# Kernel optimization log

Hardware: AMD Instinct MI355X
Metric: run time of the kernel (lower is better)

Reference implementation:

```python
import jax, jax.numpy as jnp
import numpy as np

B, S, H, D = 2, 2048, 16, 128
HID = H * D
THETA = 10000.0
SCALE = 1.0 / np.sqrt(D)


def setup_inputs() -> dict:
    key = jax.random.key(0)
    k1, k2, k3 = jax.random.split(key, 3)
    x = jax.random.normal(k1, (B, S, HID), dtype=jnp.float32)
    w_qkv = jax.random.normal(k2, (3 * HID, HID), dtype=jnp.float32) * 0.02
    w_o = jax.random.normal(k3, (HID, HID), dtype=jnp.float32) * 0.02
    return {"x": x, "w_qkv": w_qkv, "w_o": w_o}


def _rope_cos_sin(seq_len, dim, dtype):
    inv_freq = 1.0 / (THETA ** (jnp.arange(0, dim, 2, dtype=jnp.float32) / dim))
    pos = jnp.arange(seq_len, dtype=jnp.float32)
    freqs = pos[:, None] * inv_freq[None, :]          # (S, D/2)
    emb = jnp.concatenate([freqs, freqs], axis=-1)    # (S, D)
    return jnp.cos(emb).astype(dtype), jnp.sin(emb).astype(dtype)


def _rotate_half(t):
    t1, t2 = jnp.split(t, 2, axis=-1)
    return jnp.concatenate([-t2, t1], axis=-1)


def reference(x, w_qkv, w_o):
    b, s, _ = x.shape
    qkv = jnp.einsum('bsh,oh->bso', x, w_qkv)                 # (B,S,3*HID)
    qkv = qkv.reshape(b, s, 3, H, D).transpose(2, 0, 3, 1, 4)  # (3,B,H,S,D)
    q, k, v = qkv[0], qkv[1], qkv[2]
    cos, sin = _rope_cos_sin(s, D, x.dtype)                    # (S,D)
    q = q * cos + _rotate_half(q) * sin
    k = k * cos + _rotate_half(k) * sin
    scores = jnp.einsum('bhqd,bhkd->bhqk', q, k) * SCALE       # (B,H,S,S)
    causal = jnp.triu(jnp.ones((s, s), dtype=bool), k=1)
    scores = jnp.where(causal[None, None], -jnp.inf, scores)
    attn = jax.nn.softmax(scores.astype(jnp.float32), axis=-1).astype(q.dtype)
    out = jnp.einsum('bhqk,bhkd->bhqd', attn, v)               # (B,H,S,D)
    out = out.transpose(0, 2, 1, 3).reshape(b, s, HID)
    return jnp.einsum('bsh,oh->bso', out, w_o)
```

## Files before the change

kernel.cpp:

```cpp
#include <hip/hip_runtime.h>
#include <hip/hip_bf16.h>

typedef unsigned short u16;
typedef unsigned long long u64;
typedef u16 us8 __attribute__((ext_vector_type(8)));
typedef __bf16 bf8_t __attribute__((ext_vector_type(8)));
typedef float f32x4 __attribute__((ext_vector_type(4)));

__device__ __forceinline__ float b2f(u16 u) {
    return __uint_as_float(((unsigned int)u) << 16);
}
__device__ __forceinline__ u16 f2b(float f) {
    union { __hip_bfloat16 h; u16 u; } v;
    v.h = __float2bfloat16(f);
    return v.u;
}
__device__ __forceinline__ f32x4 mfma16(bf8_t a, bf8_t b, f32x4 c) {
    return __builtin_amdgcn_mfma_f32_16x16x32_bf16(a, b, c, 0, 0, 0);
}
__device__ __forceinline__ void gload_lds16(const u16* g, u16* lds_base) {
    __builtin_amdgcn_global_load_lds((const __attribute__((address_space(1))) unsigned int*)g,
                                     (__attribute__((address_space(3))) unsigned int*)lds_base,
                                     16, 0, 0);
}

__global__ __launch_bounds__(256) void f32_to_bf16(const float* __restrict__ src,
                                                   u16* __restrict__ dst, int n8) {
    int idx = blockIdx.x * 256 + threadIdx.x;
    if (idx >= n8) return;
    float4 f0 = ((const float4*)src)[idx * 2];
    float4 f1 = ((const float4*)src)[idx * 2 + 1];
    us8 o;
    o[0] = f2b(f0.x); o[1] = f2b(f0.y); o[2] = f2b(f0.z); o[3] = f2b(f0.w);
    o[4] = f2b(f1.x); o[5] = f2b(f1.y); o[6] = f2b(f1.z); o[7] = f2b(f1.w);
    ((us8*)dst)[idx] = o;
}

#define BARX() __builtin_amdgcn_s_barrier()
#define LGKM0() do { asm volatile("s_waitcnt lgkmcnt(0)" ::: "memory"); \
                     __builtin_amdgcn_sched_barrier(0); } while (0)
#define VM4A()  do { asm volatile("s_waitcnt vmcnt(4)" ::: "memory"); \
                     __builtin_amdgcn_sched_barrier(0); } while (0)

__global__ __launch_bounds__(512, 2) void gemm192(const u16* __restrict__ A,
                                                  const u16* __restrict__ B,
                                                  u16* __restrict__ Cout, int ldc) {
    __shared__ u16 LA[2][256 * 64];
    __shared__ u16 LB[2][192 * 64];

    const int tid = threadIdx.x;
    const int w = tid >> 6, lane = tid & 63;
    const int lm = lane & 15, lq = lane >> 4;
    const int wm = w >> 1, wn = w & 1;

    const int bid = blockIdx.x;
    const int nper = gridDim.x >> 3;
    const int wg = (bid & 7) * nper + (bid >> 3);
    const int mt = wg & 15, nt = wg >> 4;
    const int m0 = mt * 256, n0 = nt * 192;

    const int srow = lane >> 3;
    const int scol = ((lane & 7) ^ srow) * 8;

    const u16* Ag = A + (size_t)(m0 + srow) * 2048 + scol;
    const u16* Bg = B + (size_t)(n0 + srow) * 2048 + scol;

#define STAGE_A2(c, kt, jb) do { \
    _Pragma("unroll") \
    for (int j = 0; j < 2; j++) { \
        int R = ((jb) + j) * 64 + w * 8; \
        gload_lds16(Ag + (size_t)R * 2048 + (kt) * 64, &LA[c][R * 64]); \
    } } while (0)

#define STAGE_B3(c, kt) do { \
    _Pragma("unroll") \
    for (int j = 0; j < 3; j++) { \
        int R = j * 64 + w * 8; \
        gload_lds16(Bg + (size_t)R * 2048 + (kt) * 64, &LB[c][R * 64]); \
    } } while (0)

    bf8_t af[4][2], bfr[6][2];
    f32x4 acc[4][6] = {};
    const int cswz = (lm & 7) << 4;

#define RD_A4(c) do { \
    _Pragma("unroll") \
    for (int m = 0; m < 4; m++) \
    _Pragma("unroll") \
    for (int ks = 0; ks < 2; ks++) { \
        int row = wm * 64 + m * 16 + lm; \
        int o = (row * 128 + ks * 64 + lq * 16) ^ cswz; \
        af[m][ks] = *(const bf8_t*)((const char*)&LA[c][0] + o); \
    } } while (0)

#define RD_B2(c, np) do { \
    _Pragma("unroll") \
    for (int n = 0; n < 2; n++) \
    _Pragma("unroll") \
    for (int ks = 0; ks < 2; ks++) { \
        int row = wn * 96 + ((np) * 2 + n) * 16 + lm; \
        int o = (row * 128 + ks * 64 + lq * 16) ^ cswz; \
        bfr[(np) * 2 + n][ks] = *(const bf8_t*)((const char*)&LB[c][0] + o); \
    } } while (0)

#define QUAD6(np) do { \
    __builtin_amdgcn_s_setprio(1); \
    _Pragma("unroll") \
    for (int m = 0; m < 4; m++) \
    _Pragma("unroll") \
    for (int n = 0; n < 2; n++) \
    _Pragma("unroll") \
    for (int ks = 0; ks < 2; ks++) \
        acc[m][(np) * 2 + n] = mfma16(af[m][ks], bfr[(np) * 2 + n][ks], \
                                      acc[m][(np) * 2 + n]); \
    __builtin_amdgcn_s_setprio(0); \
    } while (0)

#define TILE192(c, tB, tA) do { \
    RD_A4(c); RD_B2(c, 0); \
    STAGE_B3((c) ^ 1, tB); \
    BARX(); LGKM0(); \
    QUAD6(0); \
    BARX(); \
    RD_B2(c, 1); \
    STAGE_A2(c, tA, 0); \
    BARX(); LGKM0(); \
    QUAD6(1); \
    BARX(); \
    RD_B2(c, 2); \
    STAGE_A2(c, tA, 2); \
    BARX(); LGKM0(); \
    QUAD6(2); \
    VM4A(); \
    BARX(); \
} while (0)

    STAGE_A2(0, 0, 0); STAGE_A2(0, 0, 2);
    STAGE_B3(0, 0);
    STAGE_A2(1, 1, 0); STAGE_A2(1, 1, 2);
    VM4A();
    BARX();

    for (int it = 0; it < 16; it++) {
        const int t0 = 2 * it, t1 = 2 * it + 1;
        const int tB0 = t1;
        const int tA0 = (t0 + 2 < 32) ? t0 + 2 : 31;
        const int tB1 = (t1 + 1 < 32) ? t1 + 1 : 31;
        const int tA1 = (t1 + 2 < 32) ? t1 + 2 : 31;
        TILE192(0, tB0, tA0);
        TILE192(1, tB1, tA1);
    }

#pragma unroll
    for (int m = 0; m < 4; m++)
#pragma unroll
        for (int n = 0; n < 6; n++)
#pragma unroll
            for (int r = 0; r < 4; r++) {
                int row = m0 + wm * 64 + m * 16 + lq * 4 + r;
                int col = n0 + wn * 96 + n * 16 + lm;
                Cout[(size_t)row * ldc + col] = f2b(acc[m][n][r]);
            }
#undef TILE192
#undef QUAD6
#undef RD_A4
#undef RD_B2
#undef STAGE_A2
#undef STAGE_B3
}

#define VMN() do { \
    asm volatile("s_waitcnt vmcnt(2)" ::: "memory"); \
    __builtin_amdgcn_sched_barrier(0); } while (0)

__global__ __launch_bounds__(512, 2) void gemm_op(const u16* __restrict__ A,
                                                  const u16* __restrict__ B,
                                                  float* __restrict__ Cout, int ldc) {
    __shared__ u16 LA[2][128 * 64];
    __shared__ u16 LB[2][256 * 64];

    const int tid = threadIdx.x;
    const int w = tid >> 6, lane = tid & 63;
    const int lm = lane & 15, lq = lane >> 4;
    const int wm = w >> 2, wn = w & 3;

    const int bid = blockIdx.x;
    const int nper = gridDim.x >> 3;
    const int wg = (bid & 7) * nper + (bid >> 3);
    const int mt = wg & 31, nt = wg >> 5;
    const int m0 = mt * 128, n0 = nt * 256;

    const int srow = lane >> 3;
    const int scol = ((lane & 7) ^ srow) * 8;

    const u16* Ag = A + (size_t)(m0 + srow) * 2048 + scol;
    const u16* Bg = B + (size_t)(n0 + srow) * 2048 + scol;

#define STAGE_A(c, h, kt) do { \
    _Pragma("unroll") \
    for (int i = 0; i < 2; i++) { \
        int R = w * 2 + i; \
        if ((h) == 0) \
            gload_lds16(Ag + (size_t)(R * 8) * 2048 + (kt) * 64, &LA[c][(R * 8) * 64]); \
    } } while (0)

#define STAGE_B(c, h, kt) do { \
    _Pragma("unroll") \
    for (int i = 0; i < 2; i++) { \
        int R = w * 2 + i; \
        gload_lds16(Bg + (size_t)((h) * 128 + R * 8) * 2048 + (kt) * 64, \
                    &LB[c][((h) * 128 + R * 8) * 64]); \
    } } while (0)

    bf8_t af[4][2], bfr[4][2];
    f32x4 acc[4][4] = {};
    const int cswz = (lm & 7) << 4;

#define RD_A(c, mh) do { \
    _Pragma("unroll") \
    for (int m = 0; m < 2; m++) \
    _Pragma("unroll") \
    for (int ks = 0; ks < 2; ks++) { \
        int row = wm * 64 + ((mh) * 2 + m) * 16 + lm; \
        int o = (row * 128 + ks * 64 + lq * 16) ^ cswz; \
        af[(mh) * 2 + m][ks] = *(const bf8_t*)((const char*)&LA[c][0] + o); \
    } } while (0)

#define RD_B(c, nh) do { \
    _Pragma("unroll") \
    for (int n = 0; n < 2; n++) \
    _Pragma("unroll") \
    for (int ks = 0; ks < 2; ks++) { \
        int row = wn * 64 + ((nh) * 2 + n) * 16 + lm; \
        int o = (row * 128 + ks * 64 + lq * 16) ^ cswz; \
        bfr[(nh) * 2 + n][ks] = *(const bf8_t*)((const char*)&LB[c][0] + o); \
    } } while (0)

#define QUAD(mh, nh) do { \
    __builtin_amdgcn_s_setprio(1); \
    _Pragma("unroll") \
    for (int m = 0; m < 2; m++) \
    _Pragma("unroll") \
    for (int n = 0; n < 2; n++) \
    _Pragma("unroll") \
    for (int ks = 0; ks < 2; ks++) \
        acc[(mh) * 2 + m][(nh) * 2 + n] = mfma16(af[(mh) * 2 + m][ks], \
            bfr[(nh) * 2 + n][ks], acc[(mh) * 2 + m][(nh) * 2 + n]); \
    __builtin_amdgcn_s_setprio(0); \
    } while (0)

#define TILEOP(c, tB, tA) do { \
    RD_A(c, 0); RD_B(c, 0); \
    STAGE_B((c) ^ 1, 0, tB); \
    BARX(); LGKM0(); \
    QUAD(0, 0); \
    BARX(); \
    RD_A(c, 1); \
    STAGE_B((c) ^ 1, 1, tB); \
    BARX(); LGKM0(); \
    QUAD(1, 0); \
    BARX(); \
    RD_B(c, 1); \
    STAGE_A(c, 0, tA); \
    BARX(); LGKM0(); \
    QUAD(0, 1); \
    BARX(); \
    QUAD(1, 1); \
    VMN(); \
    BARX(); \
} while (0)

    STAGE_A(0, 0, 0);
    STAGE_B(0, 0, 0); STAGE_B(0, 1, 0);
    STAGE_A(1, 0, 1);
    VMN();
    BARX();

    for (int it = 0; it < 16; it++) {
        const int t0 = 2 * it, t1 = 2 * it + 1;
        const int tB0 = t1;
        const int tA0 = (t0 + 2 < 32) ? t0 + 2 : 31;
        const int tB1 = (t1 + 1 < 32) ? t1 + 1 : 31;
        const int tA1 = (t1 + 2 < 32) ? t1 + 2 : 31;
        TILEOP(0, tB0, tA0);
        TILEOP(1, tB1, tA1);
    }

#pragma unroll
    for (int m = 0; m < 4; m++)
#pragma unroll
        for (int n = 0; n < 4; n++)
#pragma unroll
            for (int r = 0; r < 4; r++) {
                int row = m0 + wm * 64 + m * 16 + lq * 4 + r;
                int col = n0 + wn * 64 + n * 16 + lm;
                Cout[(size_t)row * ldc + col] = acc[m][n][r];
            }
#undef TILEOP
#undef QUAD
#undef RD_A
#undef RD_B
#undef STAGE_A
#undef STAGE_B
}

__global__ __launch_bounds__(256) void rope_vt(u16* __restrict__ qkv, u16* __restrict__ VT) {
    __shared__ u16 T[64 * 136];
    const int tid = threadIdx.x;
    const int s0 = blockIdx.x * 64;
    const int bh = blockIdx.y;
    const int b = bh >> 4, h = bh & 15;
#pragma unroll
    for (int p = 0; p < 4; p++) {
        int sl = p * 16 + (tid >> 4);
        int d0 = (tid & 15) * 8;
        *(us8*)&T[sl * 136 + d0] =
            *(const us8*)(qkv + ((size_t)(b * 2048 + s0 + sl)) * 6144 + 4096 + h * 128 + d0);
    }
#pragma unroll
    for (int p = 0; p < 2; p++) {
        int task = p * 256 + tid;
        int sl = task >> 3;
        int jg = task & 7;
        size_t base = ((size_t)(b * 2048 + s0 + sl)) * 6144 + h * 128 + jg * 8;
        us8 qlo = *(const us8*)(qkv + base);
        us8 qhi = *(const us8*)(qkv + base + 64);
        us8 klo = *(const us8*)(qkv + base + 2048);
        us8 khi = *(const us8*)(qkv + base + 2048 + 64);
        us8 oql, oqh, okl, okh;
        float s = (float)(s0 + sl);
#pragma unroll
        for (int e = 0; e < 8; e++) {
            int j = jg * 8 + e;
            float inv = __expf((float)j * (-9.210340371976184f / 64.f));
            float ang = s * inv;
            float sn, c;
            __sincosf(ang, &sn, &c);
            float q1 = b2f(qlo[e]), q2 = b2f(qhi[e]);
            oql[e] = f2b(q1 * c - q2 * sn);
            oqh[e] = f2b(q2 * c + q1 * sn);
            float k1 = b2f(klo[e]), k2 = b2f(khi[e]);
            okl[e] = f2b(k1 * c - k2 * sn);
            okh[e] = f2b(k2 * c + k1 * sn);
        }
        *(us8*)(qkv + base) = oql;
        *(us8*)(qkv + base + 64) = oqh;
        *(us8*)(qkv + base + 2048) = okl;
        *(us8*)(qkv + base + 2048 + 64) = okh;
    }
    __syncthreads();
#pragma unroll
    for (int p = 0; p < 4; p++) {
        int idx = p * 256 + tid;
        int d = idx & 127;
        int sg = idx >> 7;
        us8 v;
#pragma unroll
        for (int i = 0; i < 8; i++) v[i] = T[(sg * 8 + i) * 136 + d];
        *(us8*)&VT[((size_t)bh * 128 + d) * 2048 + s0 + sg * 8] = v;
    }
}

#define ATT_SCALE 0.08838834764831845f

__global__ __launch_bounds__(256, 2) void attn_flash(const u16* __restrict__ qkv, const u16* __restrict__ VT,
                                                     u16* __restrict__ AO) {
    const int bid = blockIdx.x;
    const int swz = (bid & 7) * 64 + (bid >> 3);
    const int bh = swz >> 4;
    const int pair = swz & 15;
    const int b = bh >> 4, h = bh & 15;
    const int tid = threadIdx.x, lane = tid & 63, wave = tid >> 6;
    const int lm = lane & 15, lq = lane >> 4;

    const int jq0 = 31 - pair;
    const int jq1 = pair;
    const int ktmax = jq0;

    __shared__ u16 Kt[64 * 136];
    __shared__ u16 Vt[128 * 72];

    bf8_t qf[2][4];
#pragma unroll
    for (int qg = 0; qg < 2; qg++) {
        const int jqv = qg ? jq1 : jq0;
        const u16* Qrow = qkv + ((size_t)(b * 2048 + jqv * 64 + wave * 16 + lm)) * 6144 + h * 128;
#pragma unroll
        for (int ks = 0; ks < 4; ks++)
            qf[qg][ks] = *(const bf8_t*)(Qrow + ks * 32 + lq * 8);
    }

    f32x4 Of[2][8] = {};
    float mrun[2] = {-3.0e38f, -3.0e38f}, lrun[2] = {0.f, 0.f};

    const u16* Kbase = qkv + (size_t)b * 2048 * 6144 + 2048 + h * 128;
    const u16* VTbase = VT + (size_t)bh * 128 * 2048;

    const int krow = tid >> 4;
    const int kcol = (tid & 15) * 8;
    const int vrow = tid >> 3;
    const int vcol = (tid & 7) * 8;

    us8 kreg[4], vreg[4];
#pragma unroll
    for (int p = 0; p < 4; p++) {
        kreg[p] = *(const us8*)(Kbase + (size_t)(p * 16 + krow) * 6144 + kcol);
        vreg[p] = *(const us8*)(VTbase + (size_t)(p * 32 + vrow) * 2048 + vcol);
    }

    for (int kt = 0; kt <= ktmax; kt++) {
        __syncthreads();
#pragma unroll
        for (int p = 0; p < 4; p++) {
            *(us8*)&Kt[(p * 16 + krow) * 136 + kcol] = kreg[p];
            *(us8*)&Vt[(p * 32 + vrow) * 72 + vcol] = vreg[p];
        }
        __syncthreads();
        {
            int kn = (kt + 1 <= ktmax ? kt + 1 : ktmax) * 64;
#pragma unroll
            for (int p = 0; p < 4; p++) {
                kreg[p] = *(const us8*)(Kbase + (size_t)(kn + p * 16 + krow) * 6144 + kcol);
                vreg[p] = *(const us8*)(VTbase + (size_t)(p * 32 + vrow) * 2048 + kn + vcol);
            }
        }

        const bool act1 = (kt <= jq1);
        u64 pk[2][4];
#pragma unroll
        for (int qg = 0; qg < 2; qg++) {
            if (qg == 0 || act1) {
                const int jqv = qg ? jq1 : jq0;
                float sv[4][4];
#pragma unroll
                for (int nb = 0; nb < 4; nb++) {
                    f32x4 a = {};
#pragma unroll
                    for (int ks = 0; ks < 4; ks++) {
                        bf8_t kf = *(const bf8_t*)&Kt[(nb * 16 + lm) * 136 + ks * 32 + lq * 8];
                        a = mfma16(kf, qf[qg][ks], a);
                    }
#pragma unroll
                    for (int r = 0; r < 4; r++) sv[nb][r] = a[r] * ATT_SCALE;
                }
                if (kt == jqv) {
                    int qglob = jqv * 64 + wave * 16 + lm;
#pragma unroll
                    for (int nb = 0; nb < 4; nb++)
#pragma unroll
                        for (int r = 0; r < 4; r++)
                            if (kt * 64 + nb * 16 + lq * 4 + r > qglob) sv[nb][r] = -3.0e38f;
                }
                float mx = -3.0e38f;
#pragma unroll
                for (int nb = 0; nb < 4; nb++)
#pragma unroll
                    for (int r = 0; r < 4; r++) mx = fmaxf(mx, sv[nb][r]);
                mx = fmaxf(mx, __shfl_xor(mx, 16, 64));
                mx = fmaxf(mx, __shfl_xor(mx, 32, 64));
                float mnew = fmaxf(mrun[qg], mx);
                float a_ = __expf(mrun[qg] - mnew);
                float rs = 0.f;
#pragma unroll
                for (int nb = 0; nb < 4; nb++) {
                    float e0 = __expf(sv[nb][0] - mnew), e1 = __expf(sv[nb][1] - mnew);
                    float e2 = __expf(sv[nb][2] - mnew), e3 = __expf(sv[nb][3] - mnew);
                    rs += (e0 + e1) + (e2 + e3);
                    unsigned int lo = (unsigned int)f2b(e0) | ((unsigned int)f2b(e1) << 16);
                    unsigned int hi = (unsigned int)f2b(e2) | ((unsigned int)f2b(e3) << 16);
                    pk[qg][nb] = (u64)lo | ((u64)hi << 32);
                }
                rs += __shfl_xor(rs, 16, 64);
                rs += __shfl_xor(rs, 32, 64);
                lrun[qg] = lrun[qg] * a_ + rs;
                mrun[qg] = mnew;
#pragma unroll
                for (int db = 0; db < 8; db++)
#pragma unroll
                    for (int r = 0; r < 4; r++) Of[qg][db][r] *= a_;
            }
        }

        const int slo = ((lq & 1) * 2) * 16 + lm;
        const int shi = slo + 16;
        const bool sel = (lq >> 1) != 0;
#pragma unroll
        for (int kk = 0; kk < 2; kk++) {
            union { u64 v[2]; bf8_t f; } pf[2];
#pragma unroll
            for (int qg = 0; qg < 2; qg++) {
                if (qg == 0 || act1) {
                    u64 lo0 = __shfl(pk[qg][2 * kk + 0], slo, 64);
                    u64 lo1 = __shfl(pk[qg][2 * kk + 1], slo, 64);
                    u64 hi0 = __shfl(pk[qg][2 * kk + 0], shi, 64);
                    u64 hi1 = __shfl(pk[qg][2 * kk + 1], shi, 64);
                    pf[qg].v[0] = sel ? lo1 : lo0;
                    pf[qg].v[1] = sel ? hi1 : hi0;
                }
            }
#pragma unroll
            for (int db = 0; db < 8; db++) {
                bf8_t vf = *(const bf8_t*)&Vt[(db * 16 + lm) * 72 + kk * 32 + lq * 8];
                Of[0][db] = mfma16(vf, pf[0].f, Of[0][db]);
                if (act1) Of[1][db] = mfma16(vf, pf[1].f, Of[1][db]);
            }
        }
    }
#pragma unroll
    for (int qg = 0; qg < 2; qg++) {
        const int jqv = qg ? jq1 : jq0;
        float invl = 1.f / lrun[qg];
        size_t rowbase = (size_t)(b * 2048 + jqv * 64 + wave * 16 + lm) * 2048 + h * 128;
#pragma unroll
        for (int db = 0; db < 8; db++) {
            ushort4 o;
            o.x = f2b(Of[qg][db][0] * invl);
            o.y = f2b(Of[qg][db][1] * invl);
            o.z = f2b(Of[qg][db][2] * invl);
            o.w = f2b(Of[qg][db][3] * invl);
            *(ushort4*)(AO + rowbase + db * 16 + lq * 4) = o;
        }
    }
}

extern "C" void kernel_launch(void* const* d_in, const int* in_sizes, int n_in,
                              void* d_out, int out_size, void* d_ws, size_t ws_size,
                              hipStream_t stream) {
    const float* x     = (const float*)d_in[0];
    const float* w_qkv = (const float*)d_in[1];
    const float* w_o   = (const float*)d_in[2];
    float* out = (float*)d_out;
    u16* ws = (u16*)d_ws;

    u16* qkvb  = ws;
    u16* VT    = ws + 25165824;
    u16* AO    = ws + 33554432;
    u16* xb    = ws + 41943040;
    u16* wqkvb = ws + 50331648;
    u16* wob   = ws + 62914560;

    f32_to_bf16<<<4096, 256, 0, stream>>>(x, xb, 1048576);
    f32_to_bf16<<<6144, 256, 0, stream>>>(w_qkv, wqkvb, 1572864);
    f32_to_bf16<<<2048, 256, 0, stream>>>(w_o, wob, 524288);
    gemm192<<<512, 512, 0, stream>>>(xb, wqkvb, qkvb, 6144);
    rope_vt<<<dim3(32, 32), 256, 0, stream>>>(qkvb, VT);
    attn_flash<<<dim3(512), 256, 0, stream>>>(qkvb, VT, AO);
    gemm_op<<<256, 512, 0, stream>>>(AO, wob, out, 2048);
}
```

Before: 380.6 us.

## Cut per-tile barriers in GEMM main loops by batching LDS reads and stages

Restructures the inner tile schedule of both GEMM kernels so that all LDS fragment reads for a tile are issued up front. The next global-to-LDS stages are grouped around a single mid-tile barrier, which replaces the three or four barrier plus lgkmcnt(0) pairs used before. The goal is to reduce workgroup synchronisation stalls and let MFMAs overlap more with memory traffic. Explicit lgkmcnt waits are removed, so correctness now depends on the compiler inserting the waits for LDS reads, and more fragments stay live in registers at once.

New measurement: 388.5 us. 2.1% more time.

```diff
diff --git a/kernel.cpp b/kernel.cpp
--- a/kernel.cpp
+++ b/kernel.cpp
@@ -37,8 +37,7 @@
 }
 
 #define BARX() __builtin_amdgcn_s_barrier()
-#define LGKM0() do { asm volatile("s_waitcnt lgkmcnt(0)" ::: "memory"); \
-                     __builtin_amdgcn_sched_barrier(0); } while (0)
+#define SBAR() __builtin_amdgcn_sched_barrier(0)
 #define VM4A()  do { asm volatile("s_waitcnt vmcnt(4)" ::: "memory"); \
                      __builtin_amdgcn_sched_barrier(0); } while (0)
 
@@ -119,17 +118,12 @@
 #define TILE192(c, tB, tA) do { \
     RD_A4(c); RD_B2(c, 0); \
     STAGE_B3((c) ^ 1, tB); \
-    BARX(); LGKM0(); \
     QUAD6(0); \
+    RD_B2(c, 1); RD_B2(c, 2); \
+    SBAR(); \
     BARX(); \
-    RD_B2(c, 1); \
-    STAGE_A2(c, tA, 0); \
-    BARX(); LGKM0(); \
+    STAGE_A2(c, tA, 0); STAGE_A2(c, tA, 2); \
     QUAD6(1); \
-    BARX(); \
-    RD_B2(c, 2); \
-    STAGE_A2(c, tA, 2); \
-    BARX(); LGKM0(); \
     QUAD6(2); \
     VM4A(); \
     BARX(); \
@@ -196,12 +190,11 @@
     const u16* Ag = A + (size_t)(m0 + srow) * 2048 + scol;
     const u16* Bg = B + (size_t)(n0 + srow) * 2048 + scol;
 
-#define STAGE_A(c, h, kt) do { \
+#define STAGE_A(c, kt) do { \
     _Pragma("unroll") \
     for (int i = 0; i < 2; i++) { \
         int R = w * 2 + i; \
-        if ((h) == 0) \
-            gload_lds16(Ag + (size_t)(R * 8) * 2048 + (kt) * 64, &LA[c][(R * 8) * 64]); \
+        gload_lds16(Ag + (size_t)(R * 8) * 2048 + (kt) * 64, &LA[c][(R * 8) * 64]); \
     } } while (0)
 
 #define STAGE_B(c, h, kt) do { \
@@ -250,29 +243,21 @@
     } while (0)
 
 #define TILEOP(c, tB, tA) do { \
-    RD_A(c, 0); RD_B(c, 0); \
-    STAGE_B((c) ^ 1, 0, tB); \
-    BARX(); LGKM0(); \
-    QUAD(0, 0); \
+    RD_A(c, 0); RD_A(c, 1); RD_B(c, 0); \
+    STAGE_B((c) ^ 1, 0, tB); STAGE_B((c) ^ 1, 1, tB); \
+    QUAD(0, 0); QUAD(1, 0); \
+    RD_B(c, 1); \
+    SBAR(); \
     BARX(); \
-    RD_A(c, 1); \
-    STAGE_B((c) ^ 1, 1, tB); \
-    BARX(); LGKM0(); \
-    QUAD(1, 0); \
-    BARX(); \
-    RD_B(c, 1); \
-    STAGE_A(c, 0, tA); \
-    BARX(); LGKM0(); \
-    QUAD(0, 1); \
-    BARX(); \
-    QUAD(1, 1); \
+    STAGE_A(c, tA); \
+    QUAD(0, 1); QUAD(1, 1); \
     VMN(); \
     BARX(); \
 } while (0)
 
-    STAGE_A(0, 0, 0);
+    STAGE_A(0, 0);
     STAGE_B(0, 0, 0); STAGE_B(0, 1, 0);
-    STAGE_A(1, 0, 1);
+    STAGE_A(1, 1);
     VMN();
     BARX();
 
```
